# Optimization experiments

Hardware: AMD Instinct MI355X
Metric: run time of the kernel (lower is better)

The kernel has to match this reference:

```python
import jax, jax.numpy as jnp
import numpy as np

N = 10000      # nodes
E = 160000     # edges
F_IN = 84
H = 256
P = 4          # powers [0,1,2,3]
L = 3          # mixhop layers


def setup_inputs() -> dict:
    key = jax.random.key(0)
    ks = jax.random.split(key, 10)
    s = 0.05
    inp = {}
    inp["x"] = jax.random.normal(ks[0], (N, F_IN), jnp.float32)
    inp["edge_index"] = jax.random.randint(ks[1], (2, E), 0, N, dtype=jnp.int32)
    inp["w_in"] = jax.random.normal(ks[2], (F_IN, H), jnp.float32) * s
    inp["b_in"] = jnp.zeros((H,), jnp.float32)
    inp["mh_w0"] = jax.random.normal(ks[3], (P, H, H), jnp.float32) * s
    inp["mh_b0"] = jnp.zeros((P, H), jnp.float32)
    inp["mh_w12"] = jax.random.normal(ks[4], (2, P, P * H, H), jnp.float32) * s
    inp["mh_b12"] = jnp.zeros((2, P, H), jnp.float32)
    inp["ln_g"] = jnp.ones((L, P * H), jnp.float32)
    inp["ln_b"] = jnp.zeros((L, P * H), jnp.float32)
    inp["w1"] = jax.random.normal(ks[5], (P * H, H), jnp.float32) * s
    inp["b1"] = jnp.zeros((H,), jnp.float32)
    inp["w2"] = jax.random.normal(ks[6], (H, H // 2), jnp.float32) * s
    inp["b2"] = jnp.zeros((H // 2,), jnp.float32)
    inp["w3"] = jax.random.normal(ks[7], (H // 2, 1), jnp.float32) * s
    inp["b3"] = jnp.zeros((1,), jnp.float32)
    return inp


def _gcn_norm(edge_index, n):
    # D^{-1/2} (A + I) D^{-1/2}, PyG gcn_norm with add_self_loops=True
    loop = jnp.arange(n, dtype=edge_index.dtype)
    src = jnp.concatenate([edge_index[0], loop])
    dst = jnp.concatenate([edge_index[1], loop])
    deg = jax.ops.segment_sum(jnp.ones(src.shape[0], jnp.float32), dst, num_segments=n)
    dinv = jnp.where(deg > 0, deg ** -0.5, 0.0)
    return src, dst, dinv[src] * dinv[dst]


def _propagate(h, src, dst, w, n):
    # out[i] = sum_{(j->i)} w_e * h[j]
    return jax.ops.segment_sum(h[src] * w[:, None], dst, num_segments=n)


def _mixhop(h, src, dst, w, n, W, B):
    outs = [h @ W[0] + B[0]]  # power 0
    for p in range(1, W.shape[0]):
        h = _propagate(h, src, dst, w, n)
        outs.append(h @ W[p] + B[p])
    return jnp.concatenate(outs, axis=-1)  # [n, P*H]


def _layernorm(x, g, b, eps=1e-5):
    mu = x.mean(-1, keepdims=True)
    var = x.var(-1, keepdims=True)
    return (x - mu) * jax.lax.rsqrt(var + eps) * g + b


def reference(x, edge_index, w_in, b_in, mh_w0, mh_b0, mh_w12, mh_b12,
              ln_g, ln_b, w1, b1, w2, b2, w3, b3):
    gelu = lambda t: jax.nn.gelu(t, approximate=False)  # torch default (erf)
    n = x.shape[0]
    src, dst, w = _gcn_norm(edge_index, n)
    h = gelu(x @ w_in + b_in)
    for i in range(L):
        W, B = (mh_w0, mh_b0) if i == 0 else (mh_w12[i - 1], mh_b12[i - 1])
        h = _mixhop(h, src, dst, w, n, W, B)
        h = gelu(_layernorm(h, ln_g[i], ln_b[i]))
        # dropout inactive at inference
    h = gelu(h @ w1 + b1)
    h = gelu(h @ w2 + b2)
    out = h @ w3 + b3
    return out.squeeze(-1)  # [N]
```

## Files before the change

### kernel.cpp

```cpp
#include <hip/hip_runtime.h>

typedef unsigned short u16;
typedef unsigned char u8;
typedef unsigned int u32;
typedef __bf16 bf16x8 __attribute__((ext_vector_type(8)));
typedef float f32x4 __attribute__((ext_vector_type(4)));
typedef float f32x2 __attribute__((ext_vector_type(2)));

#define NN 10000
#define EE 160000
#define MPAD 10112

__device__ inline float b2f(u16 u) { return __uint_as_float(((u32)u) << 16); }
__device__ inline u16 f2b(float f) {
    u32 u = __float_as_uint(f);
    return (u16)((u + 0x7fffu + ((u >> 16) & 1u)) >> 16);
}
__device__ inline u8 f2f8(float v) {
    return (u8)(__builtin_amdgcn_cvt_pk_fp8_f32(v, v, 0, false) & 0xff);
}
__device__ inline float gelu_f(float x) {
    return 0.5f * x * (1.0f + erff(x * 0.70710678118654752f));
}
__device__ inline void load_lds16(const u16* g, u16* l) {
    __builtin_amdgcn_global_load_lds((const __attribute__((address_space(1))) u32*)g,
                                     (__attribute__((address_space(3))) u32*)l, 16, 0, 0);
}

__global__ __launch_bounds__(256) void k_count(const int* __restrict__ dst, int* __restrict__ cnt) {
    int e = blockIdx.x * 256 + threadIdx.x;
    if (e < EE) atomicAdd(&cnt[dst[e]], 1);
}

__global__ __launch_bounds__(256) void k_scan(const int* __restrict__ cnt, int* __restrict__ rowptr,
                                              int* __restrict__ cursor, float* __restrict__ dinv) {
    __shared__ int part[256];
    const int t = threadIdx.x;
    const int CH = 40;
    int base = t * CH;
    int ssum = 0;
    for (int k = 0; k < CH; k++) { int i = base + k; if (i < NN) ssum += cnt[i]; }
    part[t] = ssum;
    __syncthreads();
    for (int off = 1; off < 256; off <<= 1) {
        int v = (t >= off) ? part[t - off] : 0;
        __syncthreads();
        part[t] += v;
        __syncthreads();
    }
    int run = part[t] - ssum;
    for (int k = 0; k < CH; k++) {
        int i = base + k;
        if (i < NN) {
            rowptr[i] = run; cursor[i] = run;
            int c = cnt[i];
            dinv[i] = rsqrtf((float)(c + 1));
            run += c;
        }
    }
    if (t == 255) rowptr[NN] = run;
}

__global__ __launch_bounds__(256) void k_fill(const int* __restrict__ src, const int* __restrict__ dst,
                                              int* __restrict__ cursor, int* __restrict__ cols,
                                              float* __restrict__ vals, const float* __restrict__ dinv) {
    int e = blockIdx.x * 256 + threadIdx.x;
    if (e < EE) {
        int s = src[e], d = dst[e];
        int pos = atomicAdd(&cursor[d], 1);
        cols[pos] = s;
        vals[pos] = dinv[s] * dinv[d];
    }
}

__global__ __launch_bounds__(256) void k_padx(const float* __restrict__ x, u16* __restrict__ xp) {
    int idx = blockIdx.x * 256 + threadIdx.x;
    if (idx >= MPAD * 128) return;
    int r = idx >> 7, c = idx & 127;
    u16 v = 0;
    if (r < NN && c < 84) v = f2b(x[(size_t)r * 84 + c]);
    xp[idx] = v;
}

struct TT { const float* src; u16* dst; int K, Nc, Kp; };
__global__ __launch_bounds__(256) void k_transT(TT t0, TT t1, TT t2, TT t3, TT t4) {
    int b = blockIdx.x; TT T;
    if (b < 8)        { T = t0; }
    else if (b < 72)  { T = t1; b -= 8; }
    else if (b < 584) { T = t2; b -= 72; }
    else if (b < 648) { T = t3; b -= 584; }
    else              { T = t4; b -= 648; }
    int tk = (T.Kp + 63) >> 6, tn = T.Nc >> 6;
    int bb  = b / (tk * tn);
    int rem = b - bb * (tk * tn);
    int k0 = (rem / tn) * 64, n0 = (rem % tn) * 64;
    __shared__ u16 tile[64][65];
    const float* src = T.src + (size_t)bb * T.K * T.Nc;
    u16* dst = T.dst + (size_t)bb * T.Nc * T.Kp;
    int c = threadIdx.x & 63, r0 = threadIdx.x >> 6;
#pragma unroll
    for (int i = 0; i < 16; i++) {
        int r = r0 + i * 4;
        int k = k0 + r;
        u16 v = 0;
        if (k < T.K) v = f2b(src[(size_t)k * T.Nc + n0 + c]);
        tile[r][c] = v;
    }
    __syncthreads();
    int rr = threadIdx.x & 63, cc0 = threadIdx.x >> 6;
#pragma unroll
    for (int i = 0; i < 16; i++) {
        int cc = cc0 + i * 4;
        int k = k0 + rr;
        if (k < T.Kp) dst[(size_t)(n0 + cc) * T.Kp + k] = tile[rr][cc];
    }
}

struct CvtSrcs { const float *b_in, *mh_b0, *mh_b12, *ln_g, *ln_b, *b1, *b2, *w3, *b3; };
__global__ __launch_bounds__(256) void k_cvt_all(CvtSrcs S, u16* __restrict__ dst) {
    int i = blockIdx.x * 256 + threadIdx.x;
    const float* s; int base;
    if (i < 256)       { s = S.b_in;   base = 0; }
    else if (i < 1280) { s = S.mh_b0;  base = 256; }
    else if (i < 3328) { s = S.mh_b12; base = 1280; }
    else if (i < 6400) { s = S.ln_g;   base = 3328; }
    else if (i < 9472) { s = S.ln_b;   base = 6400; }
    else if (i < 9728) { s = S.b1;     base = 9472; }
    else if (i < 9856) { s = S.b2;     base = 9728; }
    else if (i < 9984) { s = S.w3;     base = 9856; }
    else if (i < 9985) { s = S.b3;     base = 9984; }
    else return;
    dst[i] = f2b(s[i - base]);
}

template<int TM, int TN, int ACT, int EPI, int BATCH>
__global__ __launch_bounds__(256) void k_gemm(const u16* __restrict__ A0, const u16* __restrict__ A1,
                                              const u16* __restrict__ A2, const u16* __restrict__ A3,
                                              const u16* __restrict__ Bt, const u16* __restrict__ bias,
                                              u16* __restrict__ C, u8* __restrict__ Z,
                                              int K, int ldc, int col0, int NB_M, int NB_N) {
    constexpr int AM = TM / 32, AN = TN / 32;
    constexpr int CA = TM / 16, CB = TN / 16;
    constexpr int NCH = (CA + CB) / 4;
    constexpr int SLOT = (TM + TN) * 32;
    __shared__ __align__(16) u16 Sh[4][SLOT];
    int id = blockIdx.x;
    int g8 = id & 7, sIdx = id >> 3;
    int nb = sIdx % NB_N, jb = sIdx / NB_N;
    int mb = g8 + 8 * jb;
    if (mb >= NB_M) return;
    const u16* A = A0;
    if (BATCH) {
        int z = blockIdx.y;
        if (z == 1) A = A1; else if (z == 2) A = A2; else if (z == 3) A = A3;
        Bt   += (size_t)z * 256 * K;
        bias += z * 256;
        col0 += z * 256;
    }
    const int t = threadIdx.x;
    const int wv = t >> 6, lane = t & 63;
    const int wm = wv >> 1, wn = wv & 1;
    const int quad = lane >> 4, l16 = lane & 15;
    const int tileM = mb * TM, tileN = nb * TN;

    f32x4 acc[AM][AN] = {};

    const int rch = lane >> 2, c8 = (lane & 3) * 8;
    const u16* gsrc[NCH];
    int lofs[NCH];
#pragma unroll
    for (int i = 0; i < NCH; i++) {
        int c = wv + 4 * i;
        if (c < CA) {
            gsrc[i] = A + (size_t)(tileM + c * 16 + rch) * K + c8;
            lofs[i] = c * 512 + lane * 8;
        } else {
            int cc = c - CA;
            gsrc[i] = Bt + (size_t)(tileN + cc * 16 + rch) * K + c8;
            lofs[i] = TM * 32 + cc * 512 + lane * 8;
        }
    }

#pragma unroll
    for (int i = 0; i < NCH; i++) load_lds16(gsrc[i], &Sh[0][lofs[i]]);
#pragma unroll
    for (int i = 0; i < NCH; i++) load_lds16(gsrc[i] + 32, &Sh[1][lofs[i]]);

    const int npair = K >> 6;
    for (int p = 0; p < npair; p++) {
        __syncthreads();
        int cur = (p & 1) << 1;
        int nxt = cur ^ 2;
        int kc = p << 6;
        if (kc + 64 < K) {
#pragma unroll
            for (int i = 0; i < NCH; i++) load_lds16(gsrc[i] + kc + 64, &Sh[nxt][lofs[i]]);
#pragma unroll
            for (int i = 0; i < NCH; i++) load_lds16(gsrc[i] + kc + 96, &Sh[nxt + 1][lofs[i]]);
        }
#pragma unroll
        for (int h = 0; h < 2; h++) {
            const u16* S = Sh[cur + h];
            bf16x8 af[AM], bfr[AN];
#pragma unroll
            for (int tm = 0; tm < AM; tm++)
                af[tm] = *(const bf16x8*)&S[(wm * (TM / 2) + tm * 16 + l16) * 32 + quad * 8];
#pragma unroll
            for (int tn = 0; tn < AN; tn++)
                bfr[tn] = *(const bf16x8*)&S[TM * 32 + (wn * (TN / 2) + tn * 16 + l16) * 32 + quad * 8];
#pragma unroll
            for (int tm = 0; tm < AM; tm++)
#pragma unroll
                for (int tn = 0; tn < AN; tn++)
                    acc[tm][tn] = __builtin_amdgcn_mfma_f32_16x16x32_bf16(af[tm], bfr[tn], acc[tm][tn], 0, 0, 0);
        }
    }

#pragma unroll
    for (int tm = 0; tm < AM; tm++)
#pragma unroll
        for (int tn = 0; tn < AN; tn++)
#pragma unroll
            for (int r = 0; r < 4; r++) {
                int row = tileM + wm * (TM / 2) + tm * 16 + quad * 4 + r;
                int col = tileN + wn * (TN / 2) + tn * 16 + l16;
                float v = acc[tm][tn][r];
                if (EPI == 2) {
                    if (col < 256) C[(size_t)row * 1024 + col] = f2b(v + b2f(bias[col]));
                    else           Z[(size_t)row * 768 + (col - 256)] = f2f8(v);
                } else {
                    v += b2f(bias[col]);
                    if (ACT) v = gelu_f(v);
                    C[(size_t)row * ldc + col0 + col] = f2b(v);
                }
            }
}

__global__ __launch_bounds__(256) void k_propw(const u16* __restrict__ hin, int W, int G,
                                               const int* __restrict__ rowptr, const int* __restrict__ cols,
                                               const float* __restrict__ vals, const float* __restrict__ dinv,
                                               u16* __restrict__ out2) {
    int unit = blockIdx.x * 4 + (threadIdx.x >> 6);
    if (unit >= NN * G) return;
    int g = unit / NN, node = unit - g * NN;
    int lane = threadIdx.x & 63;
    int half = lane >> 5, fl = lane & 31;
    const u16* base = hin + g * 256 + fl * 8;
    float a0 = 0, a1 = 0, a2 = 0, a3 = 0, a4 = 0, a5 = 0, a6 = 0, a7 = 0;
    if (half == 1) {
        float di = dinv[node], sw = di * di;
        bf16x8 sv = *(const bf16x8*)(base + (size_t)node * W);
        a0 = sw * (float)sv[0]; a1 = sw * (float)sv[1]; a2 = sw * (float)sv[2]; a3 = sw * (float)sv[3];
        a4 = sw * (float)sv[4]; a5 = sw * (float)sv[5]; a6 = sw * (float)sv[6]; a7 = sw * (float)sv[7];
    }
    int s = rowptr[node], e = rowptr[node + 1];
    int q = s + half;
    for (; q + 6 < e; q += 8) {
        int j0 = cols[q], j1 = cols[q + 2], j2 = cols[q + 4], j3 = cols[q + 6];
        float w0 = vals[q], w1 = vals[q + 2], w2 = vals[q + 4], w3 = vals[q + 6];
        bf16x8 v0 = *(const bf16x8*)(base + (size_t)j0 * W);
        bf16x8 v1 = *(const bf16x8*)(base + (size_t)j1 * W);
        bf16x8 v2 = *(const bf16x8*)(base + (size_t)j2 * W);
        bf16x8 v3 = *(const bf16x8*)(base + (size_t)j3 * W);
        a0 += w0 * (float)v0[0] + w1 * (float)v1[0] + w2 * (float)v2[0] + w3 * (float)v3[0];
        a1 += w0 * (float)v0[1] + w1 * (float)v1[1] + w2 * (float)v2[1] + w3 * (float)v3[1];
        a2 += w0 * (float)v0[2] + w1 * (float)v1[2] + w2 * (float)v2[2] + w3 * (float)v3[2];
        a3 += w0 * (float)v0[3] + w1 * (float)v1[3] + w2 * (float)v2[3] + w3 * (float)v3[3];
        a4 += w0 * (float)v0[4] + w1 * (float)v1[4] + w2 * (float)v2[4] + w3 * (float)v3[4];
        a5 += w0 * (float)v0[5] + w1 * (float)v1[5] + w2 * (float)v2[5] + w3 * (float)v3[5];
        a6 += w0 * (float)v0[6] + w1 * (float)v1[6] + w2 * (float)v2[6] + w3 * (float)v3[6];
        a7 += w0 * (float)v0[7] + w1 * (float)v1[7] + w2 * (float)v2[7] + w3 * (float)v3[7];
    }
    for (; q < e; q += 2) {
        int j = cols[q];
        float w = vals[q];
        bf16x8 v = *(const bf16x8*)(base + (size_t)j * W);
        a0 += w * (float)v[0]; a1 += w * (float)v[1]; a2 += w * (float)v[2]; a3 += w * (float)v[3];
        a4 += w * (float)v[4]; a5 += w * (float)v[5]; a6 += w * (float)v[6]; a7 += w * (float)v[7];
    }
    a0 += __shfl_down(a0, 32); a1 += __shfl_down(a1, 32);
    a2 += __shfl_down(a2, 32); a3 += __shfl_down(a3, 32);
    a4 += __shfl_down(a4, 32); a5 += __shfl_down(a5, 32);
    a6 += __shfl_down(a6, 32); a7 += __shfl_down(a7, 32);
    if (half == 0) {
        int f = fl * 8;
        union { u16 u[8]; uint4 v; } pk;
        pk.u[0] = f2b(a0); pk.u[1] = f2b(a1); pk.u[2] = f2b(a2); pk.u[3] = f2b(a3);
        pk.u[4] = f2b(a4); pk.u[5] = f2b(a5); pk.u[6] = f2b(a6); pk.u[7] = f2b(a7);
        *(uint4*)(out2 + (size_t)node * (size_t)(G * 256) + g * 256 + f) = pk.v;
    }
}

__device__ inline void f8acc(uint2 u, float w, float* a) {
    f32x2 p0 = __builtin_amdgcn_cvt_pk_f32_fp8(u.x, false);
    f32x2 p1 = __builtin_amdgcn_cvt_pk_f32_fp8(u.x, true);
    f32x2 p2 = __builtin_amdgcn_cvt_pk_f32_fp8(u.y, false);
    f32x2 p3 = __builtin_amdgcn_cvt_pk_f32_fp8(u.y, true);
    a[0] += w * p0.x; a[1] += w * p0.y; a[2] += w * p1.x; a[3] += w * p1.y;
    a[4] += w * p2.x; a[5] += w * p2.y; a[6] += w * p3.x; a[7] += w * p3.y;
}
__global__ __launch_bounds__(256) void k_propf8(const u8* __restrict__ hin, int W, int G,
                                                const int* __restrict__ rowptr, const int* __restrict__ cols,
                                                const float* __restrict__ vals, const float* __restrict__ dinv,
                                                u16* __restrict__ concat, const u16* __restrict__ bias,
                                                int col0, u8* __restrict__ out2) {
    int unit = blockIdx.x * 4 + (threadIdx.x >> 6);
    if (unit >= NN * G) return;
    int g = unit / NN, node = unit - g * NN;
    int lane = threadIdx.x & 63;
    int half = lane >> 5, fl = lane & 31;
    const u8* base = hin + g * 256 + fl * 8;
    float a[8] = {0, 0, 0, 0, 0, 0, 0, 0};
    if (half == 1) {
        float di = dinv[node];
        uint2 sv = *(const uint2*)(base + (size_t)node * W);
        f8acc(sv, di * di, a);
    }
    int s = rowptr[node], e = rowptr[node + 1];
    int q = s + half;
    for (; q + 6 < e; q += 8) {
        int j0 = cols[q], j1 = cols[q + 2], j2 = cols[q + 4], j3 = cols[q + 6];
        float w0 = vals[q], w1 = vals[q + 2], w2 = vals[q + 4], w3 = vals[q + 6];
        uint2 v0 = *(const uint2*)(base + (size_t)j0 * W);
        uint2 v1 = *(const uint2*)(base + (size_t)j1 * W);
        uint2 v2 = *(const uint2*)(base + (size_t)j2 * W);
        uint2 v3 = *(const uint2*)(base + (size_t)j3 * W);
        f8acc(v0, w0, a); f8acc(v1, w1, a); f8acc(v2, w2, a); f8acc(v3, w3, a);
    }
    for (; q < e; q += 2) {
        uint2 v = *(const uint2*)(base + (size_t)cols[q] * W);
        f8acc(v, vals[q], a);
    }
#pragma unroll
    for (int i = 0; i < 8; i++) a[i] += __shfl_down(a[i], 32);
    if (half == 0) {
        int f = fl * 8;
        if (g == 0) {
            union { u16 u[8]; uint4 v; } pk;
#pragma unroll
            for (int i = 0; i < 8; i++) pk.u[i] = f2b(a[i] + b2f(bias[f + i]));
            *(uint4*)(concat + (size_t)node * 1024 + col0 + f) = pk.v;
        } else {
            int W2 = W - 256;
            u32 lo = __builtin_amdgcn_cvt_pk_fp8_f32(a[0], a[1], 0, false);
            lo = __builtin_amdgcn_cvt_pk_fp8_f32(a[2], a[3], lo, true);
            u32 hi = __builtin_amdgcn_cvt_pk_fp8_f32(a[4], a[5], 0, false);
            hi = __builtin_amdgcn_cvt_pk_fp8_f32(a[6], a[7], hi, true);
            uint2 o; o.x = lo; o.y = hi;
            *(uint2*)(out2 + (size_t)node * W2 + (g - 1) * 256 + f) = o;
        }
    }
}

__global__ __launch_bounds__(256) void k_ln_gelu(const u16* __restrict__ X, const u16* __restrict__ g,
                                                 const u16* __restrict__ b, u16* __restrict__ out) {
    __shared__ float red[256];
    const int row = blockIdx.x, t = threadIdx.x;
    ushort4 xv = *(const ushort4*)(X + (size_t)row * 1024 + t * 4);
    float x0 = b2f(xv.x), x1 = b2f(xv.y), x2 = b2f(xv.z), x3 = b2f(xv.w);
    red[t] = x0 + x1 + x2 + x3;
    __syncthreads();
    for (int off = 128; off; off >>= 1) {
        if (t < off) red[t] += red[t + off];
        __syncthreads();
    }
    float mu = red[0] * (1.f / 1024.f);
    __syncthreads();
    float d0 = x0 - mu, d1 = x1 - mu, d2 = x2 - mu, d3 = x3 - mu;
    red[t] = d0 * d0 + d1 * d1 + d2 * d2 + d3 * d3;
    __syncthreads();
    for (int off = 128; off; off >>= 1) {
        if (t < off) red[t] += red[t + off];
        __syncthreads();
    }
    float rs = rsqrtf(red[0] * (1.f / 1024.f) + 1e-5f);
    int c = t * 4;
    ushort4 gv = *(const ushort4*)(g + c);
    ushort4 bv = *(const ushort4*)(b + c);
    ushort4 o;
    o.x = f2b(gelu_f(d0 * rs * b2f(gv.x) + b2f(bv.x)));
    o.y = f2b(gelu_f(d1 * rs * b2f(gv.y) + b2f(bv.y)));
    o.z = f2b(gelu_f(d2 * rs * b2f(gv.z) + b2f(bv.z)));
    o.w = f2b(gelu_f(d3 * rs * b2f(gv.w) + b2f(bv.w)));
    *(ushort4*)(out + (size_t)row * 1024 + c) = o;
}

__global__ __launch_bounds__(256) void k_final(const u16* __restrict__ h, const u16* __restrict__ w3,
                                               const u16* __restrict__ b3, float* __restrict__ out) {
    int gw = (blockIdx.x * 256 + threadIdx.x) >> 6;
    int lane = threadIdx.x & 63;
    if (gw >= NN) return;
    u32 hv = *(const u32*)(h + (size_t)gw * 128 + lane * 2);
    u32 wv = *(const u32*)(w3 + lane * 2);
    float s = b2f((u16)(hv & 0xffff)) * b2f((u16)(wv & 0xffff)) +
              b2f((u16)(hv >> 16)) * b2f((u16)(wv >> 16));
    for (int off = 32; off; off >>= 1) s += __shfl_down(s, off);
    if (lane == 0) out[gw] = s + b2f(b3[0]);
}

extern "C" void kernel_launch(void* const* d_in, const int* in_sizes, int n_in,
                              void* d_out, int out_size, void* d_ws, size_t ws_size,
                              hipStream_t stream) {
    (void)in_sizes; (void)n_in; (void)out_size; (void)ws_size;
    const float* x  = (const float*)d_in[0];
    const int*   ei = (const int*)d_in[1];
    float* out = (float*)d_out;

    char* p = (char*)d_ws;
    auto alloc = [&](size_t bytes) { char* q = p; p += (bytes + 255) & ~(size_t)255; return q; };
    int*   cnt    = (int*)alloc(NN * 4);
    int*   rowptr = (int*)alloc((NN + 1) * 4);
    int*   cursor = (int*)alloc(NN * 4);
    float* dinv   = (float*)alloc(NN * 4);
    int*   cols   = (int*)alloc(EE * 4);
    float* vals   = (float*)alloc(EE * 4);
    u16*   xp     = (u16*)alloc((size_t)MPAD * 128 * 2);
    u16*   wbuf   = (u16*)alloc((size_t)2686976 * 2);
    u16*   smallC = (u16*)alloc(10240 * 2);
    u16*   S1     = (u16*)alloc((size_t)MPAD * 256 * 2);
    u16*   S2     = (u16*)alloc((size_t)MPAD * 256 * 2);
    u16*   S3     = (u16*)alloc((size_t)MPAD * 256 * 2);
    u16*   S4     = (u16*)alloc((size_t)MPAD * 256 * 2);
    u8*    Zb     = (u8*)alloc((size_t)MPAD * 768);
    u8*    Y2     = (u8*)alloc((size_t)MPAD * 512);
    u8*    Y3     = (u8*)alloc((size_t)MPAD * 256);
    u16*   bufA   = (u16*)alloc((size_t)MPAD * 1024 * 2);
    u16*   concat = (u16*)alloc((size_t)MPAD * 1024 * 2);

    u16* winT  = wbuf;
    u16* w0T   = wbuf + 32768;
    u16* w12T  = wbuf + 294912;
    u16* w1T   = wbuf + 2392064;
    u16* w2T   = wbuf + 2654208;
    u16* binC  = smallC;
    u16* mb0C  = smallC + 256;
    u16* mb12C = smallC + 1280;
    u16* lngC  = smallC + 3328;
    u16* lnbC  = smallC + 6400;
    u16* b1C   = smallC + 9472;
    u16* b2C   = smallC + 9728;
    u16* w3C   = smallC + 9856;
    u16* b3C   = smallC + 9984;

    const int* srcA = ei;
    const int* dstA = ei + EE;

    hipMemsetAsync(cnt, 0, NN * 4, stream);

    k_padx<<<(MPAD * 128 + 255) / 256, 256, 0, stream>>>(x, xp);
    TT t0{(const float*)d_in[2],  winT, 84,   256, 128};
    TT t1{(const float*)d_in[4],  w0T,  256,  256, 256};
    TT t2{(const float*)d_in[6],  w12T, 1024, 256, 1024};
    TT t3{(const float*)d_in[10], w1T,  1024, 256, 1024};
    TT t4{(const float*)d_in[12], w2T,  256,  128, 256};
    k_transT<<<656, 256, 0, stream>>>(t0, t1, t2, t3, t4);
    CvtSrcs CS{(const float*)d_in[3], (const float*)d_in[5], (const float*)d_in[7],
               (const float*)d_in[8], (const float*)d_in[9], (const float*)d_in[11],
               (const float*)d_in[13], (const float*)d_in[14], (const float*)d_in[15]};
    k_cvt_all<<<40, 256, 0, stream>>>(CS, smallC);

    k_count<<<(EE + 255) / 256, 256, 0, stream>>>(dstA, cnt);
    k_scan<<<1, 256, 0, stream>>>(cnt, rowptr, cursor, dinv);
    k_fill<<<(EE + 255) / 256, 256, 0, stream>>>(srcA, dstA, cursor, cols, vals, dinv);

    auto gx = [](int nbm, int nbn) { return 8 * ((nbm + 7) / 8) * nbn; };

    k_gemm<128, 64, 1, 0, 0><<<gx(79, 4), 256, 0, stream>>>(xp, xp, xp, xp, winT, binC, S1, nullptr, 128, 256, 0, 79, 4);

    k_propw<<<2500, 256, 0, stream>>>(S1, 256, 1, rowptr, cols, vals, dinv, S2);
    k_propw<<<2500, 256, 0, stream>>>(S2, 256, 1, rowptr, cols, vals, dinv, S3);
    k_propw<<<2500, 256, 0, stream>>>(S3, 256, 1, rowptr, cols, vals, dinv, S4);
    k_gemm<128, 64, 0, 0, 1><<<dim3(gx(79, 4), 4), 256, 0, stream>>>(S1, S2, S3, S4, w0T, mb0C, concat, nullptr, 256, 1024, 0, 79, 4);
    k_ln_gelu<<<NN, 256, 0, stream>>>(concat, lngC, lnbC, bufA);

    for (int L = 0; L < 2; L++) {
        const u16* WT = w12T + (size_t)L * 1024 * 1024;
        const u16* BB = mb12C + L * 1024;
        k_gemm<128, 64, 0, 2, 0><<<gx(79, 16), 256, 0, stream>>>(bufA, bufA, bufA, bufA, WT, BB, concat, Zb, 1024, 0, 0, 79, 16);
        k_propf8<<<7500, 256, 0, stream>>>(Zb, 768, 3, rowptr, cols, vals, dinv, concat, BB + 256, 256, Y2);
        k_propf8<<<5000, 256, 0, stream>>>(Y2, 512, 2, rowptr, cols, vals, dinv, concat, BB + 512, 512, Y3);
        k_propf8<<<2500, 256, 0, stream>>>(Y3, 256, 1, rowptr, cols, vals, dinv, concat, BB + 768, 768, nullptr);
        k_ln_gelu<<<NN, 256, 0, stream>>>(concat, lngC + (L + 1) * 1024, lnbC + (L + 1) * 1024, bufA);
    }

    k_gemm<64, 64, 1, 0, 0><<<gx(158, 4), 256, 0, stream>>>(bufA, bufA, bufA, bufA, w1T, b1C, S1, nullptr, 1024, 256, 0, 158, 4);
    k_gemm<64, 64, 1, 0, 0><<<gx(158, 2), 256, 0, stream>>>(S1, S1, S1, S1, w2T, b2C, S2, nullptr, 256, 128, 0, 158, 2);
    k_final<<<2500, 256, 0, stream>>>(S2, w3C, b3C, out);
}
```

Before: 463.7 us.

## Merge setup kernels into one ingest launch and fuse final projection into GEMM

The padding, weight transpose, small-parameter conversion and degree-count kernels are combined into one launch with block ranges dispatched by index, which removes several small launches. The last GEMM (256->128) gains an epilogue that applies bias and GELU, takes the dot product with w3 through a shuffle and shared-memory reduction, and writes the final output directly. This skips the bf16 round trip of the 128-wide hidden layer and drops the separate k_final kernel. In exchange the merged kernel carries branch divergence and reserves the transpose tile's shared memory for every block, and the last GEMM now runs with a 64x128 tile.

```diff
diff --git a/kernel.cpp b/kernel.cpp
--- a/kernel.cpp
+++ b/kernel.cpp
@@ -25,11 +25,6 @@
 __device__ inline void load_lds16(const u16* g, u16* l) {
     __builtin_amdgcn_global_load_lds((const __attribute__((address_space(1))) u32*)g,
                                      (__attribute__((address_space(3))) u32*)l, 16, 0, 0);
-}
-
-__global__ __launch_bounds__(256) void k_count(const int* __restrict__ dst, int* __restrict__ cnt) {
-    int e = blockIdx.x * 256 + threadIdx.x;
-    if (e < EE) atomicAdd(&cnt[dst[e]], 1);
 }
 
 __global__ __launch_bounds__(256) void k_scan(const int* __restrict__ cnt, int* __restrict__ rowptr,
@@ -73,64 +68,69 @@
     }
 }
 
-__global__ __launch_bounds__(256) void k_padx(const float* __restrict__ x, u16* __restrict__ xp) {
-    int idx = blockIdx.x * 256 + threadIdx.x;
-    if (idx >= MPAD * 128) return;
-    int r = idx >> 7, c = idx & 127;
-    u16 v = 0;
-    if (r < NN && c < 84) v = f2b(x[(size_t)r * 84 + c]);
-    xp[idx] = v;
-}
-
 struct TT { const float* src; u16* dst; int K, Nc, Kp; };
-__global__ __launch_bounds__(256) void k_transT(TT t0, TT t1, TT t2, TT t3, TT t4) {
-    int b = blockIdx.x; TT T;
-    if (b < 8)        { T = t0; }
-    else if (b < 72)  { T = t1; b -= 8; }
-    else if (b < 584) { T = t2; b -= 72; }
-    else if (b < 648) { T = t3; b -= 584; }
-    else              { T = t4; b -= 648; }
-    int tk = (T.Kp + 63) >> 6, tn = T.Nc >> 6;
-    int bb  = b / (tk * tn);
-    int rem = b - bb * (tk * tn);
-    int k0 = (rem / tn) * 64, n0 = (rem % tn) * 64;
-    __shared__ u16 tile[64][65];
-    const float* src = T.src + (size_t)bb * T.K * T.Nc;
-    u16* dst = T.dst + (size_t)bb * T.Nc * T.Kp;
-    int c = threadIdx.x & 63, r0 = threadIdx.x >> 6;
-#pragma unroll
-    for (int i = 0; i < 16; i++) {
-        int r = r0 + i * 4;
-        int k = k0 + r;
+struct CvtSrcs { const float *b_in, *mh_b0, *mh_b12, *ln_g, *ln_b, *b1, *b2, *w3, *b3; };
+__global__ __launch_bounds__(256) void k_ingest(TT t0, TT t1, TT t2, TT t3, TT t4,
+                                                const float* __restrict__ x, u16* __restrict__ xp,
+                                                CvtSrcs S, u16* __restrict__ smallC,
+                                                const int* __restrict__ dstA, int* __restrict__ cnt) {
+    int b = blockIdx.x;
+    const int t = threadIdx.x;
+    if (b < 656) {
+        TT T;
+        if (b < 8)        { T = t0; }
+        else if (b < 72)  { T = t1; b -= 8; }
+        else if (b < 584) { T = t2; b -= 72; }
+        else if (b < 648) { T = t3; b -= 584; }
+        else              { T = t4; b -= 648; }
+        int tk = (T.Kp + 63) >> 6, tn = T.Nc >> 6;
+        int bb  = b / (tk * tn);
+        int rem = b - bb * (tk * tn);
+        int k0 = (rem / tn) * 64, n0 = (rem % tn) * 64;
+        __shared__ u16 tile[64][65];
+        const float* src = T.src + (size_t)bb * T.K * T.Nc;
+        u16* dst = T.dst + (size_t)bb * T.Nc * T.Kp;
+        int c = t & 63, r0 = t >> 6;
+#pragma unroll
+        for (int i = 0; i < 16; i++) {
+            int r = r0 + i * 4;
+            int k = k0 + r;
+            u16 v = 0;
+            if (k < T.K) v = f2b(src[(size_t)k * T.Nc + n0 + c]);
+            tile[r][c] = v;
+        }
+        __syncthreads();
+        int rr = t & 63, cc0 = t >> 6;
+#pragma unroll
+        for (int i = 0; i < 16; i++) {
+            int cc = cc0 + i * 4;
+            int k = k0 + rr;
+            if (k < T.Kp) dst[(size_t)(n0 + cc) * T.Kp + k] = tile[rr][cc];
+        }
+    } else if (b < 5712) {
+        int idx = (b - 656) * 256 + t;
+        int r = idx >> 7, c = idx & 127;
         u16 v = 0;
-        if (k < T.K) v = f2b(src[(size_t)k * T.Nc + n0 + c]);
-        tile[r][c] = v;
-    }
-    __syncthreads();
-    int rr = threadIdx.x & 63, cc0 = threadIdx.x >> 6;
-#pragma unroll
-    for (int i = 0; i < 16; i++) {
-        int cc = cc0 + i * 4;
-        int k = k0 + rr;
-        if (k < T.Kp) dst[(size_t)(n0 + cc) * T.Kp + k] = tile[rr][cc];
-    }
-}
-
-struct CvtSrcs { const float *b_in, *mh_b0, *mh_b12, *ln_g, *ln_b, *b1, *b2, *w3, *b3; };
-__global__ __launch_bounds__(256) void k_cvt_all(CvtSrcs S, u16* __restrict__ dst) {
-    int i = blockIdx.x * 256 + threadIdx.x;
-    const float* s; int base;
-    if (i < 256)       { s = S.b_in;   base = 0; }
-    else if (i < 1280) { s = S.mh_b0;  base = 256; }
-    else if (i < 3328) { s = S.mh_b12; base = 1280; }
-    else if (i < 6400) { s = S.ln_g;   base = 3328; }
-    else if (i < 9472) { s = S.ln_b;   base = 6400; }
-    else if (i < 9728) { s = S.b1;     base = 9472; }
-    else if (i < 9856) { s = S.b2;     base = 9728; }
-    else if (i < 9984) { s = S.w3;     base = 9856; }
-    else if (i < 9985) { s = S.b3;     base = 9984; }
-    else return;
-    dst[i] = f2b(s[i - base]);
+        if (r < NN && c < 84) v = f2b(x[(size_t)r * 84 + c]);
+        xp[idx] = v;
+    } else if (b < 5752) {
+        int i = (b - 5712) * 256 + t;
+        const float* s; int base;
+        if (i < 256)       { s = S.b_in;   base = 0; }
+        else if (i < 1280) { s = S.mh_b0;  base = 256; }
+        else if (i < 3328) { s = S.mh_b12; base = 1280; }
+        else if (i < 6400) { s = S.ln_g;   base = 3328; }
+        else if (i < 9472) { s = S.ln_b;   base = 6400; }
+        else if (i < 9728) { s = S.b1;     base = 9472; }
+        else if (i < 9856) { s = S.b2;     base = 9728; }
+        else if (i < 9984) { s = S.w3;     base = 9856; }
+        else if (i < 9985) { s = S.b3;     base = 9984; }
+        else return;
+        smallC[i] = f2b(s[i - base]);
+    } else {
+        int e = (b - 5752) * 256 + t;
+        if (e < EE) atomicAdd(&cnt[dstA[e]], 1);
+    }
 }
 
 template<int TM, int TN, int ACT, int EPI, int BATCH>
@@ -138,12 +138,15 @@
                                               const u16* __restrict__ A2, const u16* __restrict__ A3,
                                               const u16* __restrict__ Bt, const u16* __restrict__ bias,
                                               u16* __restrict__ C, u8* __restrict__ Z,
+                                              const u16* __restrict__ w3c, const u16* __restrict__ b3c,
+                                              float* __restrict__ fout,
                                               int K, int ldc, int col0, int NB_M, int NB_N) {
     constexpr int AM = TM / 32, AN = TN / 32;
     constexpr int CA = TM / 16, CB = TN / 16;
     constexpr int NCH = (CA + CB) / 4;
     constexpr int SLOT = (TM + TN) * 32;
     __shared__ __align__(16) u16 Sh[4][SLOT];
+    __shared__ float shred[2][64];
     int id = blockIdx.x;
     int g8 = id & 7, sIdx = id >> 3;
     int nb = sIdx % NB_N, jb = sIdx / NB_N;
@@ -200,20 +203,43 @@
         }
 #pragma unroll
         for (int h = 0; h < 2; h++) {
-            const u16* S = Sh[cur + h];
+            const u16* Sb = Sh[cur + h];
             bf16x8 af[AM], bfr[AN];
 #pragma unroll
             for (int tm = 0; tm < AM; tm++)
-                af[tm] = *(const bf16x8*)&S[(wm * (TM / 2) + tm * 16 + l16) * 32 + quad * 8];
+                af[tm] = *(const bf16x8*)&Sb[(wm * (TM / 2) + tm * 16 + l16) * 32 + quad * 8];
 #pragma unroll
             for (int tn = 0; tn < AN; tn++)
-                bfr[tn] = *(const bf16x8*)&S[TM * 32 + (wn * (TN / 2) + tn * 16 + l16) * 32 + quad * 8];
+                bfr[tn] = *(const bf16x8*)&Sb[TM * 32 + (wn * (TN / 2) + tn * 16 + l16) * 32 + quad * 8];
 #pragma unroll
             for (int tm = 0; tm < AM; tm++)
 #pragma unroll
                 for (int tn = 0; tn < AN; tn++)
                     acc[tm][tn] = __builtin_amdgcn_mfma_f32_16x16x32_bf16(af[tm], bfr[tn], acc[tm][tn], 0, 0, 0);
         }
+    }
+
+    if (EPI == 3) {
+#pragma unroll
+        for (int tm = 0; tm < AM; tm++)
+#pragma unroll
+            for (int r = 0; r < 4; r++) {
+                float psum = 0.f;
+#pragma unroll
+                for (int tn = 0; tn < AN; tn++) {
+                    int col = wn * (TN / 2) + tn * 16 + l16;
+                    float v = gelu_f(acc[tm][tn][r] + b2f(bias[col]));
+                    psum += v * b2f(w3c[col]);
+                }
+                for (int off = 8; off; off >>= 1) psum += __shfl_down(psum, off);
+                if (l16 == 0) shred[wn][wm * (TM / 2) + tm * 16 + quad * 4 + r] = psum;
+            }
+        __syncthreads();
+        if (t < TM) {
+            int row = tileM + t;
+            if (row < NN) fout[row] = shred[0][t] + shred[1][t] + b2f(b3c[0]);
+        }
+        return;
     }
 
 #pragma unroll
@@ -383,19 +409,6 @@
     o.z = f2b(gelu_f(d2 * rs * b2f(gv.z) + b2f(bv.z)));
     o.w = f2b(gelu_f(d3 * rs * b2f(gv.w) + b2f(bv.w)));
     *(ushort4*)(out + (size_t)row * 1024 + c) = o;
-}
-
-__global__ __launch_bounds__(256) void k_final(const u16* __restrict__ h, const u16* __restrict__ w3,
-                                               const u16* __restrict__ b3, float* __restrict__ out) {
-    int gw = (blockIdx.x * 256 + threadIdx.x) >> 6;
-    int lane = threadIdx.x & 63;
-    if (gw >= NN) return;
-    u32 hv = *(const u32*)(h + (size_t)gw * 128 + lane * 2);
-    u32 wv = *(const u32*)(w3 + lane * 2);
-    float s = b2f((u16)(hv & 0xffff)) * b2f((u16)(wv & 0xffff)) +
-              b2f((u16)(hv >> 16)) * b2f((u16)(wv >> 16));
-    for (int off = 32; off; off >>= 1) s += __shfl_down(s, off);
-    if (lane == 0) out[gw] = s + b2f(b3[0]);
 }
 
 extern "C" void kernel_launch(void* const* d_in, const int* in_sizes, int n_in,
@@ -447,43 +460,44 @@
 
     hipMemsetAsync(cnt, 0, NN * 4, stream);
 
-    k_padx<<<(MPAD * 128 + 255) / 256, 256, 0, stream>>>(x, xp);
     TT t0{(const float*)d_in[2],  winT, 84,   256, 128};
     TT t1{(const float*)d_in[4],  w0T,  256,  256, 256};
     TT t2{(const float*)d_in[6],  w12T, 1024, 256, 1024};
     TT t3{(const float*)d_in[10], w1T,  1024, 256, 1024};
     TT t4{(const float*)d_in[12], w2T,  256,  128, 256};
-    k_transT<<<656, 256, 0, stream>>>(t0, t1, t2, t3, t4);
     CvtSrcs CS{(const float*)d_in[3], (const float*)d_in[5], (const float*)d_in[7],
                (const float*)d_in[8], (const float*)d_in[9], (const float*)d_in[11],
                (const float*)d_in[13], (const float*)d_in[14], (const float*)d_in[15]};
-    k_cvt_all<<<40, 256, 0, stream>>>(CS, smallC);
-
-    k_count<<<(EE + 255) / 256, 256, 0, stream>>>(dstA, cnt);
+    k_ingest<<<6377, 256, 0, stream>>>(t0, t1, t2, t3, t4, x, xp, CS, smallC, dstA, cnt);
+
     k_scan<<<1, 256, 0, stream>>>(cnt, rowptr, cursor, dinv);
     k_fill<<<(EE + 255) / 256, 256, 0, stream>>>(srcA, dstA, cursor, cols, vals, dinv);
 
     auto gx = [](int nbm, int nbn) { return 8 * ((nbm + 7) / 8) * nbn; };
 
-    k_gemm<128, 64, 1, 0, 0><<<gx(79, 4), 256, 0, stream>>>(xp, xp, xp, xp, winT, binC, S1, nullptr, 128, 256, 0, 79, 4);
+    k_gemm<128, 64, 1, 0, 0><<<gx(79, 4), 256, 0, stream>>>(xp, xp, xp, xp, winT, binC, S1, nullptr,
+                                                            nullptr, nullptr, nullptr, 128, 256, 0, 79, 4);
 
     k_propw<<<2500, 256, 0, stream>>>(S1, 256, 1, rowptr, cols, vals, dinv, S2);
     k_propw<<<2500, 256, 0, stream>>>(S2, 256, 1, rowptr, cols, vals, dinv, S3);
     k_propw<<<2500, 256, 0, stream>>>(S3, 256, 1, rowptr, cols, vals, dinv, S4);
-    k_gemm<128, 64, 0, 0, 1><<<dim3(gx(79, 4), 4), 256, 0, stream>>>(S1, S2, S3, S4, w0T, mb0C, concat, nullptr, 256, 1024, 0, 79, 4);
+    k_gemm<128, 64, 0, 0, 1><<<dim3(gx(79, 4), 4), 256, 0, stream>>>(S1, S2, S3, S4, w0T, mb0C, concat, nullptr,
+                                                                     nullptr, nullptr, nullptr, 256, 1024, 0, 79, 4);
     k_ln_gelu<<<NN, 256, 0, stream>>>(concat, lngC, lnbC, bufA);
 
     for (int L = 0; L < 2; L++) {
         const u16* WT = w12T + (size_t)L * 1024 * 1024;
         const u16* BB = mb12C + L * 1024;
-        k_gemm<128, 64, 0, 2, 0><<<gx(79, 16), 256, 0, stream>>>(bufA, bufA, bufA, bufA, WT, BB, concat, Zb, 1024, 0, 0, 79, 16);
+        k_gemm<128, 64, 0, 2, 0><<<gx(79, 16), 256, 0, stream>>>(bufA, bufA, bufA, bufA, WT, BB, concat, Zb,
+                                                                 nullptr, nullptr, nullptr, 1024, 0, 0, 79, 16);
         k_propf8<<<7500, 256, 0, stream>>>(Zb, 768, 3, rowptr, cols, vals, dinv, concat, BB + 256, 256, Y2);
         k_propf8<<<5000, 256, 0, stream>>>(Y2, 512, 2, rowptr, cols, vals, dinv, concat, BB + 512, 512, Y3);
         k_propf8<<<2500, 256, 0, stream>>>(Y3, 256, 1, rowptr, cols, vals, dinv, concat, BB + 768, 768, nullptr);
         k_ln_gelu<<<NN, 256, 0, stream>>>(concat, lngC + (L + 1) * 1024, lnbC + (L + 1) * 1024, bufA);
     }
 
-    k_gemm<64, 64, 1, 0, 0><<<gx(158, 4), 256, 0, stream>>>(bufA, bufA, bufA, bufA, w1T, b1C, S1, nullptr, 1024, 256, 0, 158, 4);
-    k_gemm<64, 64, 1, 0, 0><<<gx(158, 2), 256, 0, stream>>>(S1, S1, S1, S1, w2T, b2C, S2, nullptr, 256, 128, 0, 158, 2);
-    k_final<<<2500, 256, 0, stream>>>(S2, w3C, b3C, out);
-}
+    k_gemm<64, 64, 1, 0, 0><<<gx(158, 4), 256, 0, stream>>>(bufA, bufA, bufA, bufA, w1T, b1C, S1, nullptr,
+                                                            nullptr, nullptr, nullptr, 1024, 256, 0, 158, 4);
+    k_gemm<64, 128, 0, 3, 0><<<gx(158, 1), 256, 0, stream>>>(S1, S1, S1, S1, w2T, b2C, nullptr, nullptr,
+                                                             w3C, b3C, out, 256, 0, 0, 158, 1);
+}
```

Measured after the change: 454.1 us (median of 2 runs). 1.02x faster.
